# Optimization experiments

Hardware: AMD Instinct MI355X
Metric: run time of the kernel (lower is better)

Reference implementation:

```python
import jax, jax.numpy as jnp
import numpy as np

K = 5        # init kwarg k
GAMMA = 1.0  # init kwarg gamma
MARGIN = 2.0 # MarginRankingLoss margin


def setup_inputs() -> dict:
    key = jax.random.key(0)
    k1, k2 = jax.random.split(key)
    N, C = 8192, 256
    return {
        "input": jax.random.normal(k1, (N, C), dtype=jnp.float32),
        "target": jax.random.normal(k2, (N, C), dtype=jnp.float32),
    }


def reference(input, target):
    # cosine similarity -> negated = distance
    pred_norm = input / jnp.linalg.norm(input, axis=1, keepdims=True)
    target_norm = target / jnp.linalg.norm(target, axis=1, keepdims=True)
    dist = -jnp.matmul(pred_norm, target_norm.T)  # [N, N]
    n = dist.shape[0]
    # positive distance: diagonal (mask[i] picks only element i -> max of single elem)
    dist_ap = jnp.diagonal(dist)  # [N]
    # negatives: k smallest off-diagonal per row; exclude diagonal via +inf
    diag_mask = jnp.eye(n, dtype=bool)
    dist_off = jnp.where(diag_mask, jnp.inf, dist)
    neg_topk, _ = jax.lax.top_k(-dist_off, K)  # largest of -dist == smallest of dist
    dist_an = -neg_topk  # [N, K]
    # MarginRankingLoss(x1=dist_an, x2=gamma*dist_ap, y=1, margin=2):
    # mean(relu(-(x1 - x2) + margin))
    loss = jnp.mean(jax.nn.relu(GAMMA * dist_ap[:, None] - dist_an + MARGIN))
    return loss
```

## Files before the change

kernel.cpp:

```cpp
#include <hip/hip_runtime.h>
#include <hip/hip_bf16.h>

#define NROWS 8192
#define NC 256
#define KTOP 5
#define GAMMA 1.0f
#define MARGIN 2.0f
#define NSPLIT 8
#define PREDB 128
#define TCHUNK 64
#define CHUNKS 16
#define NSLOT (NSPLIT * 2)

typedef __bf16 bf16x8 __attribute__((ext_vector_type(8)));
typedef float f32x4 __attribute__((ext_vector_type(4)));
typedef _Float16 h2 __attribute__((ext_vector_type(2)));

static __device__ __forceinline__ void ins5pk(h2 (&t)[KTOP], h2 v) {
    t[0] = __builtin_elementwise_max(t[0], __builtin_elementwise_min(v, t[1]));
    t[1] = __builtin_elementwise_max(t[1], __builtin_elementwise_min(v, t[2]));
    t[2] = __builtin_elementwise_max(t[2], __builtin_elementwise_min(v, t[3]));
    t[3] = __builtin_elementwise_max(t[3], __builtin_elementwise_min(v, t[4]));
    t[4] = __builtin_elementwise_max(t[4], v);
}

static __device__ __forceinline__ void ins5f(float (&t)[KTOP], float v) {
    t[0] = fmaxf(t[0], fminf(v, t[1]));
    t[1] = fmaxf(t[1], fminf(v, t[2]));
    t[2] = fmaxf(t[2], fminf(v, t[3]));
    t[3] = fmaxf(t[3], fminf(v, t[4]));
    t[4] = fmaxf(t[4], v);
}

static __device__ __forceinline__ h2 pkrtz(float a, float b) {
    return __builtin_bit_cast(h2, __builtin_amdgcn_cvt_pkrtz(a, b));
}

__global__ __launch_bounds__(256) void norm_cast_kernel(
    const float* __restrict__ a, const float* __restrict__ b,
    unsigned short* __restrict__ an, unsigned short* __restrict__ bn) {
    const float* src = blockIdx.y ? b : a;
    unsigned short* dst = blockIdx.y ? bn : an;
    int row = blockIdx.x * 4 + (threadIdx.x >> 6);
    int lane = threadIdx.x & 63;
    float4 v = reinterpret_cast<const float4*>(src + (size_t)row * NC)[lane];
    float ss = v.x * v.x + v.y * v.y + v.z * v.z + v.w * v.w;
#pragma unroll
    for (int off = 32; off >= 1; off >>= 1) ss += __shfl_xor(ss, off);
    float inv = rsqrtf(ss);
    __hip_bfloat16 h0 = __float2bfloat16(v.x * inv);
    __hip_bfloat16 h1 = __float2bfloat16(v.y * inv);
    __hip_bfloat16 h2v = __float2bfloat16(v.z * inv);
    __hip_bfloat16 h3 = __float2bfloat16(v.w * inv);
    ushort4 o;
    o.x = __builtin_bit_cast(unsigned short, h0);
    o.y = __builtin_bit_cast(unsigned short, h1);
    o.z = __builtin_bit_cast(unsigned short, h2v);
    o.w = __builtin_bit_cast(unsigned short, h3);
    reinterpret_cast<ushort4*>(dst + (size_t)row * NC)[lane] = o;
}

__global__ __launch_bounds__(512, 4) void simtop_kernel(
    const unsigned short* __restrict__ predn,
    const unsigned short* __restrict__ targn,
    float* __restrict__ diag, float* __restrict__ top5p) {
    __shared__ unsigned short tb[2][TCHUNK][NC];

    int tid = threadIdx.x, w = tid >> 6, lane = tid & 63;
    int l15 = lane & 15, lq = lane >> 4;
    int id = blockIdx.x;
    int split = id & 7, bi = id >> 3;
    int pg = w >> 1, tg = w & 1;
    int pgbase = bi * PREDB + pg * 32;
    int ts0 = split * (CHUNKS * TCHUNK);

    f32x4 pb0[8], pb1[8];
    {
        const unsigned short* pp = predn + (size_t)(pgbase + l15) * NC + lq * 8;
#pragma unroll
        for (int kk = 0; kk < 8; ++kk) {
            pb0[kk] = *reinterpret_cast<const f32x4*>(pp + kk * 32);
            pb1[kk] = *reinterpret_cast<const f32x4*>(pp + 16 * NC + kk * 32);
        }
    }
#pragma unroll
    for (int kk = 0; kk < 8; ++kk)
        asm volatile("" : "+v"(pb0[kk]), "+v"(pb1[kk]));

    h2 t01[KTOP];
    h2 NEG = {(_Float16)-65504.f, (_Float16)-65504.f};
#pragma unroll
    for (int j = 0; j < KTOP; ++j) t01[j] = NEG;

    bool dblk = (split == (bi >> 3));
    int doffs = bi * PREDB + pg * 32 - ts0;
    int cdiag = doffs >> 6;
    int tgdiag = (doffs >> 5) & 1;

    const char* tgbase = (const char*)(targn + (size_t)ts0 * NC);

    f32x4 sreg[4];
#define STAGE_LOAD(c)                                                       \
    {                                                                       \
        const char* src_ = tgbase + (size_t)(c) * (TCHUNK * NC * 2);        \
        _Pragma("unroll") for (int it = 0; it < 4; ++it) sreg[it] =         \
            *reinterpret_cast<const f32x4*>(src_ + it * 8192 + tid * 16);   \
    }
#define STAGE_STORE(pbuf)                                                   \
    {                                                                       \
        _Pragma("unroll") for (int it = 0; it < 4; ++it) {                  \
            int L_ = it * 8192 + tid * 16;                                  \
            int r_ = L_ >> 9, slot_ = (L_ >> 4) & 31;                       \
            *reinterpret_cast<f32x4*>(                                      \
                &tb[pbuf][r_][(slot_ ^ (r_ & 7)) << 3]) = sreg[it];         \
        }                                                                   \
    }

    STAGE_LOAD(0);
    STAGE_STORE(0);
    __syncthreads();

    int r0 = tg * 32 + l15, r1 = r0 + 16;
    int sw0 = r0 & 7;

    for (int c = 0; c < CHUNKS; ++c) {
        int pbuf = c & 1;
        if (c + 1 < CHUNKS) STAGE_LOAD(c + 1);

        f32x4 z = {0.f, 0.f, 0.f, 0.f};
        f32x4 acc00 = z, acc01 = z, acc10 = z, acc11 = z;
#pragma unroll
        for (int kk = 0; kk < 8; ++kk) {
            bf16x8 a0 = *reinterpret_cast<const bf16x8*>(
                &tb[pbuf][r0][(((kk << 2) + lq) ^ sw0) << 3]);
            bf16x8 a1 = *reinterpret_cast<const bf16x8*>(
                &tb[pbuf][r1][(((kk << 2) + lq) ^ sw0) << 3]);
            acc00 = __builtin_amdgcn_mfma_f32_16x16x32_bf16(
                a0, __builtin_bit_cast(bf16x8, pb0[kk]), acc00, 0, 0, 0);
            acc10 = __builtin_amdgcn_mfma_f32_16x16x32_bf16(
                a0, __builtin_bit_cast(bf16x8, pb1[kk]), acc10, 0, 0, 0);
            acc01 = __builtin_amdgcn_mfma_f32_16x16x32_bf16(
                a1, __builtin_bit_cast(bf16x8, pb0[kk]), acc01, 0, 0, 0);
            acc11 = __builtin_amdgcn_mfma_f32_16x16x32_bf16(
                a1, __builtin_bit_cast(bf16x8, pb1[kk]), acc11, 0, 0, 0);
        }

        int trowbase = ts0 + c * TCHUNK + tg * 32;
        if (__builtin_expect(dblk && c == cdiag && tg == tgdiag, 0)) {
            int pc0 = pgbase + l15, pc1 = pgbase + 16 + l15;
#pragma unroll
            for (int rg = 0; rg < 2; ++rg)
#pragma unroll
                for (int j = 0; j < 4; ++j) {
                    int tr = trowbase + rg * 16 + lq * 4 + j;
                    float v0 = (rg ? acc01 : acc00)[j];
                    float v1 = (rg ? acc11 : acc10)[j];
                    if (tr == pc0) { diag[pc0] = v0; v0 = -65504.f; }
                    if (tr == pc1) { diag[pc1] = v1; v1 = -65504.f; }
                    ins5pk(t01, pkrtz(v0, v1));
                }
        } else {
#pragma unroll
            for (int rg = 0; rg < 2; ++rg)
#pragma unroll
                for (int j = 0; j < 4; ++j) {
                    float v0 = (rg ? acc01 : acc00)[j];
                    float v1 = (rg ? acc11 : acc10)[j];
                    ins5pk(t01, pkrtz(v0, v1));
                }
        }

        if (c + 1 < CHUNKS) STAGE_STORE(pbuf ^ 1);
        __syncthreads();
    }

#pragma unroll
    for (int m = 16; m <= 32; m <<= 1) {
        h2 pv[KTOP];
#pragma unroll
        for (int j = 0; j < KTOP; ++j) {
            int x = __shfl_xor(__builtin_bit_cast(int, t01[j]), m);
            pv[j] = __builtin_bit_cast(h2, x);
        }
#pragma unroll
        for (int j = 0; j < KTOP; ++j) ins5pk(t01, pv[j]);
    }

    if (lq == 0) {
        int slot = split * 2 + tg;
#pragma unroll
        for (int j = 0; j < KTOP; ++j) {
            float* base = top5p + (size_t)(slot * KTOP + j) * NROWS;
            base[pgbase + l15] = (float)t01[j].x;
            base[pgbase + 16 + l15] = (float)t01[j].y;
        }
    }
}

__global__ __launch_bounds__(256) void finalize_kernel(
    const float* __restrict__ diag, const float* __restrict__ top5p,
    float* __restrict__ out) {
    int row = blockIdx.x * 256 + threadIdx.x;
    float t5[KTOP];
#pragma unroll
    for (int j = 0; j < KTOP; ++j) t5[j] = -1e30f;
#pragma unroll 16
    for (int sj = 0; sj < NSLOT * KTOP; ++sj)
        ins5f(t5, top5p[(size_t)sj * NROWS + row]);
    float d = diag[row];
    float sum = 0.f;
#pragma unroll
    for (int j = 0; j < KTOP; ++j)
        sum += fmaxf(t5[j] - GAMMA * d + MARGIN, 0.f);
#pragma unroll
    for (int off = 32; off >= 1; off >>= 1) sum += __shfl_xor(sum, off);
    __shared__ float red[4];
    int wv = threadIdx.x >> 6;
    if ((threadIdx.x & 63) == 0) red[wv] = sum;
    __syncthreads();
    if (threadIdx.x == 0) {
        float tot = red[0] + red[1] + red[2] + red[3];
        atomicAdd(out, tot * (1.0f / ((float)NROWS * KTOP)));
    }
}

extern "C" void kernel_launch(void* const* d_in, const int* in_sizes, int n_in,
                              void* d_out, int out_size, void* d_ws,
                              size_t ws_size, hipStream_t stream) {
    (void)in_sizes; (void)n_in; (void)out_size; (void)ws_size;
    const float* input = (const float*)d_in[0];
    const float* target = (const float*)d_in[1];
    char* ws = (char*)d_ws;
    unsigned short* predn = (unsigned short*)ws;
    unsigned short* targn = (unsigned short*)(ws + (size_t)NROWS * NC * 2);
    float* diag = (float*)(ws + (size_t)NROWS * NC * 4);
    float* top5p = (float*)(ws + (size_t)NROWS * NC * 4 + NROWS * 4);
    float* out = (float*)d_out;

    (void)hipMemsetAsync(d_out, 0, sizeof(float), stream);

    dim3 gA(NROWS / 4, 2);
    norm_cast_kernel<<<gA, 256, 0, stream>>>(input, target, predn, targn);

    simtop_kernel<<<512, 512, 0, stream>>>(predn, targn, diag, top5p);

    finalize_kernel<<<NROWS / 256, 256, 0, stream>>>(diag, top5p, out);
}
```

Before: 118.1 us.

## Deepen target staging to two register sets and use lightweight barriers

Global loads of target chunks now run two chunks ahead, using two register staging sets and a loop unrolled by two. The __syncthreads calls become a waitcnt on LDS traffic plus s_barrier wrapped in sched_barrier, and the MFMA section runs at raised wave priority. Launch bounds drop from 4 to 2 blocks per CU so the extra staging registers fit. The goal is to hide global-load latency better, at the cost of higher register use and possibly lower occupancy.

```diff
diff --git a/kernel.cpp b/kernel.cpp
--- a/kernel.cpp
+++ b/kernel.cpp
@@ -60,7 +60,7 @@
     reinterpret_cast<ushort4*>(dst + (size_t)row * NC)[lane] = o;
 }
 
-__global__ __launch_bounds__(512, 4) void simtop_kernel(
+__global__ __launch_bounds__(512, 2) void simtop_kernel(
     const unsigned short* __restrict__ predn,
     const unsigned short* __restrict__ targn,
     float* __restrict__ diag, float* __restrict__ top5p) {
@@ -99,36 +99,37 @@
 
     const char* tgbase = (const char*)(targn + (size_t)ts0 * NC);
 
-    f32x4 sreg[4];
-#define STAGE_LOAD(c)                                                       \
+    f32x4 sregA[4], sregB[4];
+#define STAGE_LOAD_TO(sr, c)                                                \
     {                                                                       \
         const char* src_ = tgbase + (size_t)(c) * (TCHUNK * NC * 2);        \
-        _Pragma("unroll") for (int it = 0; it < 4; ++it) sreg[it] =         \
+        _Pragma("unroll") for (int it = 0; it < 4; ++it) sr[it] =           \
             *reinterpret_cast<const f32x4*>(src_ + it * 8192 + tid * 16);   \
     }
-#define STAGE_STORE(pbuf)                                                   \
+#define STAGE_STORE_FROM(sr, pb_)                                           \
     {                                                                       \
         _Pragma("unroll") for (int it = 0; it < 4; ++it) {                  \
             int L_ = it * 8192 + tid * 16;                                  \
             int r_ = L_ >> 9, slot_ = (L_ >> 4) & 31;                       \
             *reinterpret_cast<f32x4*>(                                      \
-                &tb[pbuf][r_][(slot_ ^ (r_ & 7)) << 3]) = sreg[it];         \
+                &tb[pb_][r_][(slot_ ^ (r_ & 7)) << 3]) = sr[it];            \
         }                                                                   \
     }
-
-    STAGE_LOAD(0);
-    STAGE_STORE(0);
-    __syncthreads();
+#define BAR()                                                               \
+    {                                                                       \
+        asm volatile("s_waitcnt lgkmcnt(0)" ::: "memory");                  \
+        __builtin_amdgcn_sched_barrier(0);                                  \
+        __builtin_amdgcn_s_barrier();                                       \
+        __builtin_amdgcn_sched_barrier(0);                                  \
+    }
 
     int r0 = tg * 32 + l15, r1 = r0 + 16;
     int sw0 = r0 & 7;
 
-    for (int c = 0; c < CHUNKS; ++c) {
-        int pbuf = c & 1;
-        if (c + 1 < CHUNKS) STAGE_LOAD(c + 1);
-
+    auto docompute = [&](int c, int pbuf) {
         f32x4 z = {0.f, 0.f, 0.f, 0.f};
         f32x4 acc00 = z, acc01 = z, acc10 = z, acc11 = z;
+        __builtin_amdgcn_s_setprio(1);
 #pragma unroll
         for (int kk = 0; kk < 8; ++kk) {
             bf16x8 a0 = *reinterpret_cast<const bf16x8*>(
@@ -144,6 +145,7 @@
             acc11 = __builtin_amdgcn_mfma_f32_16x16x32_bf16(
                 a1, __builtin_bit_cast(bf16x8, pb1[kk]), acc11, 0, 0, 0);
         }
+        __builtin_amdgcn_s_setprio(0);
 
         int trowbase = ts0 + c * TCHUNK + tg * 32;
         if (__builtin_expect(dblk && c == cdiag && tg == tgdiag, 0)) {
@@ -169,9 +171,22 @@
                     ins5pk(t01, pkrtz(v0, v1));
                 }
         }
-
-        if (c + 1 < CHUNKS) STAGE_STORE(pbuf ^ 1);
-        __syncthreads();
+    };
+
+    STAGE_LOAD_TO(sregA, 0);
+    STAGE_LOAD_TO(sregB, 1);
+    STAGE_STORE_FROM(sregA, 0);
+    BAR();
+
+    for (int c = 0; c < CHUNKS; c += 2) {
+        if (c + 2 < CHUNKS) STAGE_LOAD_TO(sregA, c + 2);
+        docompute(c, 0);
+        STAGE_STORE_FROM(sregB, 1);
+        BAR();
+        if (c + 3 < CHUNKS) STAGE_LOAD_TO(sregB, c + 3);
+        docompute(c + 1, 1);
+        if (c + 2 < CHUNKS) STAGE_STORE_FROM(sregA, 0);
+        BAR();
     }
 
 #pragma unroll
```

Result: no change. 119.8 us (+1.4%).

## Enlarge per-wave pred tile to 64 rows, remap splits by XCD, store fp16 partials

Applied to the files above, without the earlier changes.

Each wave now holds 64 pred rows in registers (pinned to AGPRs) and processes 32-row target chunks, doubling MFMA work per LDS read. Blocks are remapped so the 32 target splits are spread across XCDs, with 512 pred rows per block. Partial top-5 results are written as fp16, and s_setprio is raised around the MFMA loop. Diagonal handling is rewritten to match the new tiling. The larger register footprint may lower occupancy, and there are now more partial slots for finalize to merge.

```diff
diff --git a/kernel.cpp b/kernel.cpp
--- a/kernel.cpp
+++ b/kernel.cpp
@@ -6,11 +6,11 @@
 #define KTOP 5
 #define GAMMA 1.0f
 #define MARGIN 2.0f
-#define NSPLIT 8
-#define PREDB 128
-#define TCHUNK 64
-#define CHUNKS 16
-#define NSLOT (NSPLIT * 2)
+#define NSPLIT 32
+#define PREDB 512
+#define TCHUNK 32
+#define CHUNKS 8
+#define NSLOT NSPLIT
 
 typedef __bf16 bf16x8 __attribute__((ext_vector_type(8)));
 typedef float f32x4 __attribute__((ext_vector_type(4)));
@@ -60,68 +60,72 @@
     reinterpret_cast<ushort4*>(dst + (size_t)row * NC)[lane] = o;
 }
 
-__global__ __launch_bounds__(512, 4) void simtop_kernel(
+__global__ __launch_bounds__(512) void simtop_kernel(
     const unsigned short* __restrict__ predn,
     const unsigned short* __restrict__ targn,
-    float* __restrict__ diag, float* __restrict__ top5p) {
+    float* __restrict__ diag, _Float16* __restrict__ top5p) {
     __shared__ unsigned short tb[2][TCHUNK][NC];
 
     int tid = threadIdx.x, w = tid >> 6, lane = tid & 63;
     int l15 = lane & 15, lq = lane >> 4;
     int id = blockIdx.x;
-    int split = id & 7, bi = id >> 3;
-    int pg = w >> 1, tg = w & 1;
-    int pgbase = bi * PREDB + pg * 32;
+    int xcd = id & 7, bi = (id >> 3) & 15, hi = id >> 7;
+    int split = xcd * 4 + hi;
+    int pgbase = bi * PREDB + w * 64;
     int ts0 = split * (CHUNKS * TCHUNK);
 
-    f32x4 pb0[8], pb1[8];
+    f32x4 pb0[8], pb1[8], pb2[8], pb3[8];
     {
         const unsigned short* pp = predn + (size_t)(pgbase + l15) * NC + lq * 8;
 #pragma unroll
         for (int kk = 0; kk < 8; ++kk) {
             pb0[kk] = *reinterpret_cast<const f32x4*>(pp + kk * 32);
             pb1[kk] = *reinterpret_cast<const f32x4*>(pp + 16 * NC + kk * 32);
+            pb2[kk] = *reinterpret_cast<const f32x4*>(pp + 32 * NC + kk * 32);
+            pb3[kk] = *reinterpret_cast<const f32x4*>(pp + 48 * NC + kk * 32);
         }
     }
 #pragma unroll
     for (int kk = 0; kk < 8; ++kk)
-        asm volatile("" : "+v"(pb0[kk]), "+v"(pb1[kk]));
-
-    h2 t01[KTOP];
+        asm volatile("" : "+a"(pb0[kk]), "+a"(pb1[kk]), "+a"(pb2[kk]),
+                          "+a"(pb3[kk]));
+
+    h2 t01[KTOP], t23[KTOP];
     h2 NEG = {(_Float16)-65504.f, (_Float16)-65504.f};
 #pragma unroll
-    for (int j = 0; j < KTOP; ++j) t01[j] = NEG;
-
-    bool dblk = (split == (bi >> 3));
-    int doffs = bi * PREDB + pg * 32 - ts0;
-    int cdiag = doffs >> 6;
-    int tgdiag = (doffs >> 5) & 1;
+    for (int j = 0; j < KTOP; ++j) {
+        t01[j] = NEG;
+        t23[j] = NEG;
+    }
+
+    bool dblk = (bi == (split >> 1));
 
     const char* tgbase = (const char*)(targn + (size_t)ts0 * NC);
 
-    f32x4 sreg[4];
+    f32x4 sreg0, sreg1;
 #define STAGE_LOAD(c)                                                       \
     {                                                                       \
         const char* src_ = tgbase + (size_t)(c) * (TCHUNK * NC * 2);        \
-        _Pragma("unroll") for (int it = 0; it < 4; ++it) sreg[it] =         \
-            *reinterpret_cast<const f32x4*>(src_ + it * 8192 + tid * 16);   \
-    }
-#define STAGE_STORE(pbuf)                                                   \
+        sreg0 = *reinterpret_cast<const f32x4*>(src_ + tid * 16);           \
+        sreg1 = *reinterpret_cast<const f32x4*>(src_ + 8192 + tid * 16);    \
+    }
+#define STAGE_STORE(pb_)                                                    \
     {                                                                       \
-        _Pragma("unroll") for (int it = 0; it < 4; ++it) {                  \
-            int L_ = it * 8192 + tid * 16;                                  \
-            int r_ = L_ >> 9, slot_ = (L_ >> 4) & 31;                       \
-            *reinterpret_cast<f32x4*>(                                      \
-                &tb[pbuf][r_][(slot_ ^ (r_ & 7)) << 3]) = sreg[it];         \
-        }                                                                   \
+        int L0_ = tid * 16, L1_ = 8192 + tid * 16;                          \
+        int r0_ = L0_ >> 9, s0_ = (L0_ >> 4) & 31;                          \
+        int r1_ = L1_ >> 9, s1_ = (L1_ >> 4) & 31;                          \
+        *reinterpret_cast<f32x4*>(&tb[pb_][r0_][(s0_ ^ (r0_ & 7)) << 3]) =  \
+            sreg0;                                                          \
+        *reinterpret_cast<f32x4*>(&tb[pb_][r1_][(s1_ ^ (r1_ & 7)) << 3]) =  \
+            sreg1;                                                          \
     }
 
     STAGE_LOAD(0);
     STAGE_STORE(0);
     __syncthreads();
 
-    int r0 = tg * 32 + l15, r1 = r0 + 16;
-    int sw0 = r0 & 7;
+    int r0 = l15, r1 = l15 + 16;
+    int sw0 = l15 & 7;
 
     for (int c = 0; c < CHUNKS; ++c) {
         int pbuf = c & 1;
@@ -129,6 +133,8 @@
 
         f32x4 z = {0.f, 0.f, 0.f, 0.f};
         f32x4 acc00 = z, acc01 = z, acc10 = z, acc11 = z;
+        f32x4 acc20 = z, acc21 = z, acc30 = z, acc31 = z;
+        __builtin_amdgcn_s_setprio(1);
 #pragma unroll
         for (int kk = 0; kk < 8; ++kk) {
             bf16x8 a0 = *reinterpret_cast<const bf16x8*>(
@@ -137,37 +143,49 @@
                 &tb[pbuf][r1][(((kk << 2) + lq) ^ sw0) << 3]);
             acc00 = __builtin_amdgcn_mfma_f32_16x16x32_bf16(
                 a0, __builtin_bit_cast(bf16x8, pb0[kk]), acc00, 0, 0, 0);
+            acc01 = __builtin_amdgcn_mfma_f32_16x16x32_bf16(
+                a1, __builtin_bit_cast(bf16x8, pb0[kk]), acc01, 0, 0, 0);
             acc10 = __builtin_amdgcn_mfma_f32_16x16x32_bf16(
                 a0, __builtin_bit_cast(bf16x8, pb1[kk]), acc10, 0, 0, 0);
-            acc01 = __builtin_amdgcn_mfma_f32_16x16x32_bf16(
-                a1, __builtin_bit_cast(bf16x8, pb0[kk]), acc01, 0, 0, 0);
             acc11 = __builtin_amdgcn_mfma_f32_16x16x32_bf16(
                 a1, __builtin_bit_cast(bf16x8, pb1[kk]), acc11, 0, 0, 0);
-        }
-
-        int trowbase = ts0 + c * TCHUNK + tg * 32;
-        if (__builtin_expect(dblk && c == cdiag && tg == tgdiag, 0)) {
-            int pc0 = pgbase + l15, pc1 = pgbase + 16 + l15;
-#pragma unroll
-            for (int rg = 0; rg < 2; ++rg)
-#pragma unroll
-                for (int j = 0; j < 4; ++j) {
-                    int tr = trowbase + rg * 16 + lq * 4 + j;
-                    float v0 = (rg ? acc01 : acc00)[j];
-                    float v1 = (rg ? acc11 : acc10)[j];
-                    if (tr == pc0) { diag[pc0] = v0; v0 = -65504.f; }
-                    if (tr == pc1) { diag[pc1] = v1; v1 = -65504.f; }
-                    ins5pk(t01, pkrtz(v0, v1));
+            acc20 = __builtin_amdgcn_mfma_f32_16x16x32_bf16(
+                a0, __builtin_bit_cast(bf16x8, pb2[kk]), acc20, 0, 0, 0);
+            acc21 = __builtin_amdgcn_mfma_f32_16x16x32_bf16(
+                a1, __builtin_bit_cast(bf16x8, pb2[kk]), acc21, 0, 0, 0);
+            acc30 = __builtin_amdgcn_mfma_f32_16x16x32_bf16(
+                a0, __builtin_bit_cast(bf16x8, pb3[kk]), acc30, 0, 0, 0);
+            acc31 = __builtin_amdgcn_mfma_f32_16x16x32_bf16(
+                a1, __builtin_bit_cast(bf16x8, pb3[kk]), acc31, 0, 0, 0);
+        }
+        __builtin_amdgcn_s_setprio(0);
+
+        int u = ((split & 1) << 3) + c;
+        if (__builtin_expect(dblk && (u >> 1) == w, 0)) {
+            int h = u & 1;
+#pragma unroll
+            for (int j = 0; j < 4; ++j) {
+                if (l15 == lq * 4 + j) {
+                    if (h == 0) {
+                        diag[pgbase + l15] = acc00[j];
+                        acc00[j] = -65504.f;
+                        diag[pgbase + 16 + l15] = acc11[j];
+                        acc11[j] = -65504.f;
+                    } else {
+                        diag[pgbase + 32 + l15] = acc20[j];
+                        acc20[j] = -65504.f;
+                        diag[pgbase + 48 + l15] = acc31[j];
+                        acc31[j] = -65504.f;
+                    }
                 }
-        } else {
-#pragma unroll
-            for (int rg = 0; rg < 2; ++rg)
-#pragma unroll
-                for (int j = 0; j < 4; ++j) {
-                    float v0 = (rg ? acc01 : acc00)[j];
-                    float v1 = (rg ? acc11 : acc10)[j];
-                    ins5pk(t01, pkrtz(v0, v1));
-                }
+            }
+        }
+#pragma unroll
+        for (int j = 0; j < 4; ++j) {
+            ins5pk(t01, pkrtz(acc00[j], acc10[j]));
+            ins5pk(t01, pkrtz(acc01[j], acc11[j]));
+            ins5pk(t23, pkrtz(acc20[j], acc30[j]));
+            ins5pk(t23, pkrtz(acc21[j], acc31[j]));
         }
 
         if (c + 1 < CHUNKS) STAGE_STORE(pbuf ^ 1);
@@ -176,37 +194,43 @@
 
 #pragma unroll
     for (int m = 16; m <= 32; m <<= 1) {
-        h2 pv[KTOP];
+        h2 pv[KTOP], qv[KTOP];
 #pragma unroll
         for (int j = 0; j < KTOP; ++j) {
-            int x = __shfl_xor(__builtin_bit_cast(int, t01[j]), m);
-            pv[j] = __builtin_bit_cast(h2, x);
-        }
-#pragma unroll
-        for (int j = 0; j < KTOP; ++j) ins5pk(t01, pv[j]);
+            pv[j] = __builtin_bit_cast(
+                h2, __shfl_xor(__builtin_bit_cast(int, t01[j]), m));
+            qv[j] = __builtin_bit_cast(
+                h2, __shfl_xor(__builtin_bit_cast(int, t23[j]), m));
+        }
+#pragma unroll
+        for (int j = 0; j < KTOP; ++j) {
+            ins5pk(t01, pv[j]);
+            ins5pk(t23, qv[j]);
+        }
     }
 
     if (lq == 0) {
-        int slot = split * 2 + tg;
 #pragma unroll
         for (int j = 0; j < KTOP; ++j) {
-            float* base = top5p + (size_t)(slot * KTOP + j) * NROWS;
-            base[pgbase + l15] = (float)t01[j].x;
-            base[pgbase + 16 + l15] = (float)t01[j].y;
+            _Float16* base = top5p + (size_t)(split * KTOP + j) * NROWS;
+            base[pgbase + l15] = t01[j].x;
+            base[pgbase + 16 + l15] = t01[j].y;
+            base[pgbase + 32 + l15] = t23[j].x;
+            base[pgbase + 48 + l15] = t23[j].y;
         }
     }
 }
 
 __global__ __launch_bounds__(256) void finalize_kernel(
-    const float* __restrict__ diag, const float* __restrict__ top5p,
+    const float* __restrict__ diag, const _Float16* __restrict__ top5p,
     float* __restrict__ out) {
     int row = blockIdx.x * 256 + threadIdx.x;
     float t5[KTOP];
 #pragma unroll
     for (int j = 0; j < KTOP; ++j) t5[j] = -1e30f;
-#pragma unroll 16
+#pragma unroll 8
     for (int sj = 0; sj < NSLOT * KTOP; ++sj)
-        ins5f(t5, top5p[(size_t)sj * NROWS + row]);
+        ins5f(t5, (float)top5p[(size_t)sj * NROWS + row]);
     float d = diag[row];
     float sum = 0.f;
 #pragma unroll
@@ -234,7 +258,8 @@
     unsigned short* predn = (unsigned short*)ws;
     unsigned short* targn = (unsigned short*)(ws + (size_t)NROWS * NC * 2);
     float* diag = (float*)(ws + (size_t)NROWS * NC * 4);
-    float* top5p = (float*)(ws + (size_t)NROWS * NC * 4 + NROWS * 4);
+    _Float16* top5p =
+        (_Float16*)(ws + (size_t)NROWS * NC * 4 + NROWS * 4);
     float* out = (float*)d_out;
 
     (void)hipMemsetAsync(d_out, 0, sizeof(float), stream);
```

After: 131.5 us. 1.11x slower.
